# Performance work log

Hardware: AMD Instinct MI355X
Metric: run time of the kernel (lower is better)

The kernel has to match this reference:

```python
import jax, jax.numpy as jnp
import numpy as np

B, S, D, H, G = 16, 512, 1024, 128, 256  # batch, seq, lstm_in, lstm_hidden, gat_dim

def _linear(x, W, b):
    return x @ W.T + b

def _lstm_dir(xs, Wih, Whh, bih, bhh, reverse):
    # xs: [S, B, Din] -> hs: [S, B, H]; PyTorch gate order i, f, g, o
    b = bih + bhh
    def step(carry, xt):
        h, c = carry
        z = xt @ Wih.T + h @ Whh.T + b
        i, f, g, o = jnp.split(z, 4, axis=-1)
        c = jax.nn.sigmoid(f) * c + jax.nn.sigmoid(i) * jnp.tanh(g)
        h = jax.nn.sigmoid(o) * jnp.tanh(c)
        return (h, c), h
    init = (jnp.zeros((xs.shape[1], Whh.shape[1]), xs.dtype),
            jnp.zeros((xs.shape[1], Whh.shape[1]), xs.dtype))
    _, hs = jax.lax.scan(step, init, xs, reverse=reverse)
    return hs

def _forward(x, adj,
             l0f_Wih, l0f_Whh, l0f_bih, l0f_bhh, l0b_Wih, l0b_Whh, l0b_bih, l0b_bhh,
             l1f_Wih, l1f_Whh, l1f_bih, l1f_bhh, l1b_Wih, l1b_Whh, l1b_bih, l1b_bhh,
             fc1_W, fc1_b, wattn_W, wattn_b, lin0_W, lin0_b, lin1_W, lin1_b,
             linf_W, linf_b, fcA_W, fcA_b, fcB_W, fcB_b, fcC_W, fcC_b):
    # ---- 2-layer bidirectional LSTM ----
    xs = jnp.swapaxes(x, 0, 1)  # [S, B, D]
    h0 = jnp.concatenate([_lstm_dir(xs, l0f_Wih, l0f_Whh, l0f_bih, l0f_bhh, False),
                          _lstm_dir(xs, l0b_Wih, l0b_Whh, l0b_bih, l0b_bhh, True)], axis=-1)
    h1 = jnp.concatenate([_lstm_dir(h0, l1f_Wih, l1f_Whh, l1f_bih, l1f_bhh, False),
                          _lstm_dir(h0, l1b_Wih, l1b_Whh, l1b_bih, l1b_bhh, True)], axis=-1)
    out_lstm = jnp.swapaxes(h1, 0, 1)  # [B, S, 2H]
    # ---- GAT on fc1(x) ----
    g = _linear(x, fc1_W, fc1_b)  # [B, S, G]
    idx = jnp.arange(S)
    adj = adj.at[:, idx, idx].set(1.0)
    eye = 1e-05 * jnp.eye(S, dtype=x.dtype)
    for l in range(4):
        g0 = g
        q = _linear(g, wattn_W[l], wattn_b[l])
        a = jax.nn.sigmoid(jnp.einsum('bij,bkj->bik', q, g)) + eye
        a = a * adj
        a = a / jnp.sum(a, axis=2, keepdims=True)
        g = jnp.einsum('bij,bjd->bid', a, g)
        g = jax.nn.relu(_linear(g, lin0_W[l], lin0_b[l]))
        g = jax.nn.relu(_linear(g, lin1_W[l], lin1_b[l]))
        g = g + g0
    g = _linear(g, linf_W, linf_b)
    # ---- head (dropout in eval mode -> identity) ----
    hidden = jnp.mean(jnp.concatenate([out_lstm, g], axis=2), axis=1)  # [B, 512]
    y = jax.nn.leaky_relu(_linear(hidden, fcA_W, fcA_b), 0.1)
    y = jax.nn.leaky_relu(_linear(y, fcB_W, fcB_b), 0.1)
    y = _linear(y, fcC_W, fcC_b)  # [B, 2]
    return y, hidden


def setup_inputs() -> dict:
    key = jax.random.key(0)
    ks = jax.random.split(key, 40)
    r = lambda k, shape: jax.random.normal(k, shape, jnp.float32) * 0.05
    inp = {}
    inp['x'] = jax.random.normal(ks[0], (B, S, D), jnp.float32)
    inp['adj'] = (jax.random.uniform(ks[1], (B, S, S)) < 0.05).astype(jnp.float32)
    # LSTM params: layer0 input D, layer1 input 2H; forward/backward directions
    inp['l0f_Wih'] = r(ks[2], (4 * H, D)); inp['l0f_Whh'] = r(ks[3], (4 * H, H))
    inp['l0f_bih'] = r(ks[4], (4 * H,));  inp['l0f_bhh'] = r(ks[5], (4 * H,))
    inp['l0b_Wih'] = r(ks[6], (4 * H, D)); inp['l0b_Whh'] = r(ks[7], (4 * H, H))
    inp['l0b_bih'] = r(ks[8], (4 * H,));  inp['l0b_bhh'] = r(ks[9], (4 * H,))
    inp['l1f_Wih'] = r(ks[10], (4 * H, 2 * H)); inp['l1f_Whh'] = r(ks[11], (4 * H, H))
    inp['l1f_bih'] = r(ks[12], (4 * H,)); inp['l1f_bhh'] = r(ks[13], (4 * H,))
    inp['l1b_Wih'] = r(ks[14], (4 * H, 2 * H)); inp['l1b_Whh'] = r(ks[15], (4 * H, H))
    inp['l1b_bih'] = r(ks[16], (4 * H,)); inp['l1b_bhh'] = r(ks[17], (4 * H,))
    inp['fc1_W'] = r(ks[18], (G, D)); inp['fc1_b'] = r(ks[19], (G,))
    inp['wattn_W'] = r(ks[20], (4, G, G)); inp['wattn_b'] = r(ks[21], (4, G))
    inp['lin0_W'] = r(ks[22], (4, G, G)); inp['lin0_b'] = r(ks[23], (4, G))
    inp['lin1_W'] = r(ks[24], (4, G, G)); inp['lin1_b'] = r(ks[25], (4, G))
    inp['linf_W'] = r(ks[26], (G, G)); inp['linf_b'] = r(ks[27], (G,))
    inp['fcA_W'] = r(ks[28], (128, 512)); inp['fcA_b'] = r(ks[29], (128,))
    inp['fcB_W'] = r(ks[30], (32, 128)); inp['fcB_b'] = r(ks[31], (32,))
    inp['fcC_W'] = r(ks[32], (2, 32)); inp['fcC_b'] = r(ks[33], (2,))
    return inp


def reference(x, adj,
              l0f_Wih, l0f_Whh, l0f_bih, l0f_bhh, l0b_Wih, l0b_Whh, l0b_bih, l0b_bhh,
              l1f_Wih, l1f_Whh, l1f_bih, l1f_bhh, l1b_Wih, l1b_Whh, l1b_bih, l1b_bhh,
              fc1_W, fc1_b, wattn_W, wattn_b, lin0_W, lin0_b, lin1_W, lin1_b,
              linf_W, linf_b, fcA_W, fcA_b, fcB_W, fcB_b, fcC_W, fcC_b):
    return _forward(x, adj,
                    l0f_Wih, l0f_Whh, l0f_bih, l0f_bhh, l0b_Wih, l0b_Whh, l0b_bih, l0b_bhh,
                    l1f_Wih, l1f_Whh, l1f_bih, l1f_bhh, l1b_Wih, l1b_Whh, l1b_bih, l1b_bhh,
                    fc1_W, fc1_b, wattn_W, wattn_b, lin0_W, lin0_b, lin1_W, lin1_b,
                    linf_W, linf_b, fcA_W, fcA_b, fcB_W, fcB_b, fcC_W, fcC_b)
```

## Files before the change

### kernel.cpp

```cpp
#include <hip/hip_runtime.h>
#include <stdint.h>

#define B_ 16
#define S_ 512
#define D_ 1024
#define H4 512
#define G_ 256

typedef unsigned short u16;
using short8 = __attribute__((ext_vector_type(8))) short;
using f32x4  = __attribute__((ext_vector_type(4))) float;

__device__ __forceinline__ u16 f2bf(float f){
  unsigned int u = __float_as_uint(f);
  u += 0x7fffu + ((u >> 16) & 1u);
  return (u16)(u >> 16);
}
__device__ __forceinline__ float bf2f(u16 h){
  return __uint_as_float(((unsigned int)h) << 16);
}

struct CvtSegs {
  const float4* src[14];
  short4* dst[14];
  int blk0[15];
};
__global__ __launch_bounds__(256) void cvt_multi(CvtSegs cs){
  int blk = blockIdx.x;
  int s = 0;
  #pragma unroll
  for (int k = 0; k < 14; ++k) if (cs.blk0[k + 1] <= blk) s = k + 1;
  int i = (blk - cs.blk0[s]) * 256 + threadIdx.x;
  float4 v = cs.src[s][i];
  short4 o;
  o.x = (short)f2bf(v.x); o.y = (short)f2bf(v.y);
  o.z = (short)f2bf(v.z); o.w = (short)f2bf(v.w);
  cs.dst[s][i] = o;
}

__global__ __launch_bounds__(256) void bias_prep(const float* a,const float* b,const float* c,const float* d,
                                                 const float* e,const float* f,const float* g,const float* h,
                                                 float* out){
  int i = blockIdx.x * 256 + threadIdx.x;
  if (i >= 2048) return;
  int p = i >> 9, k = i & 511;
  const float* x1 = (p==0)?a:(p==1)?c:(p==2)?e:g;
  const float* x2 = (p==0)?b:(p==1)?d:(p==2)?f:h;
  out[i] = x1[k] + x2[k];
}

template<int ACT, bool OUT_BF16, int PERM, bool RESID>
__device__ __forceinline__ void gemm_bt_body(
    const u16* __restrict__ A, const u16* __restrict__ W,
    const float* __restrict__ bias, const u16* __restrict__ resid,
    void* __restrict__ outp, int M, int N, int K,
    long sA, long sW, long sO, int bx, int by, int bz)
{
  const u16* Ab = A + (long)bz * sA;
  const u16* Wb = W + (long)bz * sW;
  const int bm0 = by * 64, bn0 = bx * 64;
  const int tid = threadIdx.x;
  const int l = tid & 63, wid = tid >> 6;
  const int wm = (wid >> 1) * 32, wn = (wid & 1) * 32;
  const int lr = l & 15, lk8 = (l >> 4) * 8;

  const f32x4 z4 = {0.f, 0.f, 0.f, 0.f};
  f32x4 acc[2][2] = {{z4, z4}, {z4, z4}};

  const u16* Ap0 = Ab + (long)(bm0 + wm + lr) * K + lk8;
  const u16* Wp0 = Wb + (long)(bn0 + wn + lr) * K + lk8;
  for (int k0 = 0; k0 < K; k0 += 32) {
    short8 a0 = *reinterpret_cast<const short8*>(Ap0 + k0);
    short8 a1 = *reinterpret_cast<const short8*>(Ap0 + (long)16 * K + k0);
    short8 b0 = *reinterpret_cast<const short8*>(Wp0 + k0);
    short8 b1 = *reinterpret_cast<const short8*>(Wp0 + (long)16 * K + k0);
    acc[0][0] = __builtin_amdgcn_mfma_f32_16x16x32_bf16(a0, b0, acc[0][0], 0, 0, 0);
    acc[0][1] = __builtin_amdgcn_mfma_f32_16x16x32_bf16(a0, b1, acc[0][1], 0, 0, 0);
    acc[1][0] = __builtin_amdgcn_mfma_f32_16x16x32_bf16(a1, b0, acc[1][0], 0, 0, 0);
    acc[1][1] = __builtin_amdgcn_mfma_f32_16x16x32_bf16(a1, b1, acc[1][1], 0, 0, 0);
  }
  #pragma unroll
  for (int mt = 0; mt < 2; ++mt)
  #pragma unroll
  for (int nt = 0; nt < 2; ++nt) {
    int n = bn0 + wn + 16 * nt + lr;
    float bv = bias ? bias[n] : 0.f;
    #pragma unroll
    for (int r = 0; r < 4; ++r) {
      int m = bm0 + wm + 16 * mt + (l >> 4) * 4 + r;
      float v = acc[mt][nt][r] + bv;
      if (ACT == 1) v = fmaxf(v, 0.f);
      if (RESID) v += bf2f(resid[(long)m * N + n]);
      long oi;
      if (PERM == 2) {
        int t = m & 511, b = m >> 9;
        oi = (long)((t * 16 + b) * 128 + (n & 127)) * 4 + (n >> 7);
      } else {
        oi = (long)bz * sO + (long)m * N + n;
      }
      if (OUT_BF16) ((u16*)outp)[oi] = f2bf(v);
      else          ((float*)outp)[oi] = v;
    }
  }
}

template<int ACT, bool OUT_BF16, int PERM, bool RESID>
__global__ __launch_bounds__(256) void gemm_bt(
    const u16* __restrict__ A, const u16* __restrict__ W,
    const float* __restrict__ bias, const u16* __restrict__ resid,
    void* __restrict__ outp, int M, int N, int K,
    long sA, long sW, long sO)
{
  gemm_bt_body<ACT, OUT_BF16, PERM, RESID>(A, W, bias, resid, outp, M, N, K,
                                           sA, sW, sO, blockIdx.x, blockIdx.y, blockIdx.z);
}

__device__ __forceinline__ void gemm_bt_body8(
    const u16* __restrict__ A, const u16* __restrict__ W,
    const float* __restrict__ bias, u16* __restrict__ out,
    int N, int K, int bx, int by)
{
  const int bm0 = by * 64, bn0 = bx * 128;
  const int tid = threadIdx.x;
  const int l = tid & 63, wid = tid >> 6;
  const int wm = (wid >> 2) * 32, wn = (wid & 3) * 32;
  const int lr = l & 15, lk8 = (l >> 4) * 8;

  const f32x4 z4 = {0.f, 0.f, 0.f, 0.f};
  f32x4 acc[2][2] = {{z4, z4}, {z4, z4}};

  const u16* Ap0 = A + (long)(bm0 + wm + lr) * K + lk8;
  const u16* Wp0 = W + (long)(bn0 + wn + lr) * K + lk8;
  for (int k0 = 0; k0 < K; k0 += 32) {
    short8 a0 = *reinterpret_cast<const short8*>(Ap0 + k0);
    short8 a1 = *reinterpret_cast<const short8*>(Ap0 + (long)16 * K + k0);
    short8 b0 = *reinterpret_cast<const short8*>(Wp0 + k0);
    short8 b1 = *reinterpret_cast<const short8*>(Wp0 + (long)16 * K + k0);
    acc[0][0] = __builtin_amdgcn_mfma_f32_16x16x32_bf16(a0, b0, acc[0][0], 0, 0, 0);
    acc[0][1] = __builtin_amdgcn_mfma_f32_16x16x32_bf16(a0, b1, acc[0][1], 0, 0, 0);
    acc[1][0] = __builtin_amdgcn_mfma_f32_16x16x32_bf16(a1, b0, acc[1][0], 0, 0, 0);
    acc[1][1] = __builtin_amdgcn_mfma_f32_16x16x32_bf16(a1, b1, acc[1][1], 0, 0, 0);
  }
  #pragma unroll
  for (int mt = 0; mt < 2; ++mt)
  #pragma unroll
  for (int nt = 0; nt < 2; ++nt) {
    int n = bn0 + wn + 16 * nt + lr;
    float bv = bias[n];
    #pragma unroll
    for (int r = 0; r < 4; ++r) {
      int m = bm0 + wm + 16 * mt + (l >> 4) * 4 + r;
      out[(long)m * N + n] = f2bf(acc[mt][nt][r] + bv);
    }
  }
}

__device__ __forceinline__ void lstm_scan7_body(
    const float* __restrict__ X, const u16* __restrict__ Whh,
    u16* __restrict__ Hout, int dir, int bg)
{
  __shared__ __align__(16) u16 h_lds[16 * 136];
  __shared__ float z_lds[2 * 516];

  const int tid = threadIdx.x;
  const int l = tid & 63, w = tid >> 6;
  const int lr = l & 15, lk = l >> 4;

  short8 bfrag[4][4];
  #pragma unroll
  for (int nt = 0; nt < 4; ++nt)
    #pragma unroll
    for (int ks = 0; ks < 4; ++ks)
      bfrag[nt][ks] = *reinterpret_cast<const short8*>(
          Whh + (64 * w + 16 * nt + lr) * 128 + 32 * ks + 8 * lk);

  for (int i = tid; i < 16 * 136; i += 512) h_lds[i] = 0;

  const int j  = tid & 127;
  const int bq = tid >> 7;
  float c = 0.f;
  float4 xA, xB, xC, xD;

  __syncthreads();

  auto loadX = [&](int t) -> float4 {
    int ta = dir ? (S_ - 1 - t) : t;
    return *reinterpret_cast<const float4*>(X + (size_t)((ta * 16 + bg + bq) * 128 + j) * 4);
  };
  if (bq < 2) { xA = loadX(0); xB = loadX(1); xC = loadX(2); }

  const f32x4 z4 = {0.f, 0.f, 0.f, 0.f};

  auto step = [&](int t, float4& xc, float4& xt, int tload) {
    short8 af[4];
    #pragma unroll
    for (int ks = 0; ks < 4; ++ks)
      af[ks] = *reinterpret_cast<const short8*>(h_lds + lr * 136 + 32 * ks + 8 * lk);
    f32x4 acc[4] = {z4, z4, z4, z4};
    #pragma unroll
    for (int nt = 0; nt < 4; ++nt)
      #pragma unroll
      for (int ks = 0; ks < 4; ++ks)
        acc[nt] = __builtin_amdgcn_mfma_f32_16x16x32_bf16(af[ks], bfrag[nt][ks], acc[nt], 0, 0, 0);
    if (lk == 0) {
      #pragma unroll
      for (int nt = 0; nt < 4; ++nt)
        #pragma unroll
        for (int r = 0; r < 2; ++r)
          z_lds[r * 516 + 64 * w + 16 * nt + lr] = acc[nt][r];
    }
    if (bq < 2 && tload < S_) xt = loadX(tload);
    asm volatile("s_waitcnt lgkmcnt(0)" ::: "memory");
    __builtin_amdgcn_s_barrier();
    if (bq < 2) {
      int ta = dir ? (S_ - 1 - t) : t;
      float zi = z_lds[bq * 516 + j      ] + xc.x;
      float zf = z_lds[bq * 516 + 128 + j] + xc.y;
      float zg = z_lds[bq * 516 + 256 + j] + xc.z;
      float zo = z_lds[bq * 516 + 384 + j] + xc.w;
      float si = __fdividef(1.f, 1.f + __expf(-zi));
      float sf = __fdividef(1.f, 1.f + __expf(-zf));
      float so = __fdividef(1.f, 1.f + __expf(-zo));
      float eg = __expf(2.f * zg);
      float tg = 1.f - __fdividef(2.f, eg + 1.f);
      c = sf * c + si * tg;
      float ec = __expf(2.f * c);
      float tc = 1.f - __fdividef(2.f, ec + 1.f);
      float hv = so * tc;
      u16 hb = f2bf(hv);
      h_lds[bq * 136 + j] = hb;
      Hout[((size_t)(bg + bq) * S_ + ta) * 256 + dir * 128 + j] = hb;
    }
    asm volatile("s_waitcnt lgkmcnt(0)" ::: "memory");
    __builtin_amdgcn_s_barrier();
  };

  for (int t = 0; t < S_; t += 4) {
    step(t,     xA, xD, t + 3);
    step(t + 1, xB, xA, t + 4);
    step(t + 2, xC, xB, t + 5);
    step(t + 3, xD, xC, t + 6);
  }
}

__global__ __launch_bounds__(512, 1) void scan_fused(
    const float* __restrict__ Xf, const float* __restrict__ Xb,
    const u16* __restrict__ Whhf, const u16* __restrict__ Whhb,
    u16* __restrict__ Hout,
    const u16* __restrict__ gA, const u16* __restrict__ gW,
    const float* __restrict__ gb, u16* __restrict__ gOut, int gK)
{
  if (blockIdx.x < 16) {
    int dir = blockIdx.x & 1, bg = (blockIdx.x >> 1) * 2;
    lstm_scan7_body(dir ? Xb : Xf, dir ? Whhb : Whhf, Hout, dir, bg);
  } else {
    int bi = blockIdx.x - 16;
    gemm_bt_body8(gA, gW, gb, gOut, 256, gK, bi & 1, bi >> 1);
  }
}

__global__ __launch_bounds__(256) void attn_norm(
    const float* __restrict__ sc, const float* __restrict__ adj, u16* __restrict__ abf)
{
  int bz = blockIdx.y;
  int i = blockIdx.x * 4 + (threadIdx.x >> 6);
  int l = threadIdx.x & 63;
  const float* srow = sc  + ((long)bz * 512 + i) * 512;
  const float* arow = adj + ((long)bz * 512 + i) * 512;
  float av[8]; float sum = 0.f;
  #pragma unroll
  for (int k = 0; k < 8; ++k) {
    int jj = l + 64 * k;
    float sg = __fdividef(1.f, 1.f + __expf(-srow[jj]));
    float v = (jj == i) ? (sg + 1e-5f) : sg * arow[jj];
    av[k] = v; sum += v;
  }
  #pragma unroll
  for (int off = 32; off; off >>= 1) sum += __shfl_xor(sum, off);
  float r = __fdividef(1.f, sum);
  u16* orow = abf + ((long)bz * 512 + i) * 512;
  #pragma unroll
  for (int k = 0; k < 8; ++k) orow[l + 64 * k] = f2bf(av[k] * r);
}

__global__ __launch_bounds__(256) void transpose_g(const u16* __restrict__ in, u16* __restrict__ out)
{
  __shared__ u16 tile[32][33];
  int bz = blockIdx.z;
  int s0 = blockIdx.x * 32, d0 = blockIdx.y * 32;
  int tx = threadIdx.x & 31, ty = threadIdx.x >> 5;
  const u16* ip = in + (long)bz * 512 * 256;
  u16* op = out + (long)bz * 256 * 512;
  #pragma unroll
  for (int k = 0; k < 32; k += 8) tile[ty + k][tx] = ip[(long)(s0 + ty + k) * 256 + d0 + tx];
  __syncthreads();
  #pragma unroll
  for (int k = 0; k < 32; k += 8) op[(long)(d0 + ty + k) * 512 + s0 + tx] = tile[tx][ty + k];
}

__global__ __launch_bounds__(256) void mean_cat(
    const u16* __restrict__ lstm, const u16* __restrict__ gf, float* __restrict__ dout)
{
  int b = blockIdx.x;
  for (int cc = threadIdx.x; cc < 512; cc += 256) {
    const u16* src = (cc < 256) ? (lstm + (long)b * 512 * 256 + cc)
                                : (gf   + (long)b * 512 * 256 + (cc - 256));
    float s = 0.f;
    for (int t = 0; t < 512; ++t) s += bf2f(src[(long)t * 256]);
    dout[32 + b * 512 + cc] = s * (1.f / 512.f);
  }
}

__global__ __launch_bounds__(256) void head_kernel(
    const float* __restrict__ hidden,
    const float* __restrict__ fcA_W, const float* __restrict__ fcA_b,
    const float* __restrict__ fcB_W, const float* __restrict__ fcB_b,
    const float* __restrict__ fcC_W, const float* __restrict__ fcC_b,
    float* __restrict__ y)
{
  __shared__ float hb[16 * 512];
  __shared__ float ab[16 * 128];
  __shared__ float bb[16 * 32];
  int tid = threadIdx.x;
  for (int i = tid; i < 8192; i += 256) hb[i] = hidden[i];
  __syncthreads();
  for (int o = tid; o < 2048; o += 256) {
    int b = o >> 7, jj = o & 127;
    float acc = fcA_b[jj];
    const float* wrow = fcA_W + jj * 512;
    const float* hrow = hb + b * 512;
    for (int k = 0; k < 512; ++k) acc += hrow[k] * wrow[k];
    ab[o] = acc > 0.f ? acc : 0.1f * acc;
  }
  __syncthreads();
  for (int o = tid; o < 512; o += 256) {
    int b = o >> 5, jj = o & 31;
    float acc = fcB_b[jj];
    for (int k = 0; k < 128; ++k) acc += ab[b * 128 + k] * fcB_W[jj * 128 + k];
    bb[o] = acc > 0.f ? acc : 0.1f * acc;
  }
  __syncthreads();
  if (tid < 32) {
    int b = tid >> 1, jj = tid & 1;
    float acc = fcC_b[jj];
    for (int k = 0; k < 32; ++k) acc += bb[b * 32 + k] * fcC_W[jj * 32 + k];
    y[b * 2 + jj] = acc;
  }
}

extern "C" void kernel_launch(void* const* d_in, const int* in_sizes, int n_in,
                              void* d_out, int out_size, void* d_ws, size_t ws_size,
                              hipStream_t stream)
{
  const float* x       = (const float*)d_in[0];
  const float* adj     = (const float*)d_in[1];
  const float* l0f_Wih = (const float*)d_in[2];
  const float* l0f_Whh = (const float*)d_in[3];
  const float* l0f_bih = (const float*)d_in[4];
  const float* l0f_bhh = (const float*)d_in[5];
  const float* l0b_Wih = (const float*)d_in[6];
  const float* l0b_Whh = (const float*)d_in[7];
  const float* l0b_bih = (const float*)d_in[8];
  const float* l0b_bhh = (const float*)d_in[9];
  const float* l1f_Wih = (const float*)d_in[10];
  const float* l1f_Whh = (const float*)d_in[11];
  const float* l1f_bih = (const float*)d_in[12];
  const float* l1f_bhh = (const float*)d_in[13];
  const float* l1b_Wih = (const float*)d_in[14];
  const float* l1b_Whh = (const float*)d_in[15];
  const float* l1b_bih = (const float*)d_in[16];
  const float* l1b_bhh = (const float*)d_in[17];
  const float* fc1_W   = (const float*)d_in[18];
  const float* fc1_b   = (const float*)d_in[19];
  const float* wattn_W = (const float*)d_in[20];
  const float* wattn_b = (const float*)d_in[21];
  const float* lin0_W  = (const float*)d_in[22];
  const float* lin0_b  = (const float*)d_in[23];
  const float* lin1_W  = (const float*)d_in[24];
  const float* lin1_b  = (const float*)d_in[25];
  const float* linf_W  = (const float*)d_in[26];
  const float* linf_b  = (const float*)d_in[27];
  const float* fcA_W   = (const float*)d_in[28];
  const float* fcA_b   = (const float*)d_in[29];
  const float* fcB_W   = (const float*)d_in[30];
  const float* fcB_b   = (const float*)d_in[31];
  const float* fcC_W   = (const float*)d_in[32];
  const float* fcC_b   = (const float*)d_in[33];

  char* wp = (char*)d_ws;
  auto alloc = [&](size_t n) -> void* { void* p = wp; wp += (n + 255) & ~(size_t)255; return p; };

  u16* x_bf     = (u16*)alloc((size_t)B_ * S_ * D_ * 2);
  u16* w0f_ih   = (u16*)alloc((size_t)512 * 1024 * 2);
  u16* w0b_ih   = (u16*)alloc((size_t)512 * 1024 * 2);
  u16* w1f_ih   = (u16*)alloc((size_t)512 * 256 * 2);
  u16* w1b_ih   = (u16*)alloc((size_t)512 * 256 * 2);
  u16* w0f_hh   = (u16*)alloc((size_t)512 * 128 * 2);
  u16* w0b_hh   = (u16*)alloc((size_t)512 * 128 * 2);
  u16* w1f_hh   = (u16*)alloc((size_t)512 * 128 * 2);
  u16* w1b_hh   = (u16*)alloc((size_t)512 * 128 * 2);
  u16* wfc1     = (u16*)alloc((size_t)256 * 1024 * 2);
  u16* wattn_bf = (u16*)alloc((size_t)4 * 256 * 256 * 2);
  u16* wlin0_bf = (u16*)alloc((size_t)4 * 256 * 256 * 2);
  u16* wlin1_bf = (u16*)alloc((size_t)4 * 256 * 256 * 2);
  u16* wlinf_bf = (u16*)alloc((size_t)256 * 256 * 2);
  float* bias4  = (float*)alloc((size_t)2048 * 4);
  float* X0f    = (float*)alloc((size_t)S_ * 16 * 512 * 4);
  float* X0b    = (float*)alloc((size_t)S_ * 16 * 512 * 4);
  u16* h0       = (u16*)alloc((size_t)B_ * S_ * 256 * 2);
  u16* lstm_out = (u16*)alloc((size_t)B_ * S_ * 256 * 2);
  u16* gA       = (u16*)alloc((size_t)B_ * S_ * 256 * 2);
  u16* gB       = (u16*)alloc((size_t)B_ * S_ * 256 * 2);
  u16* qb       = (u16*)alloc((size_t)B_ * S_ * 256 * 2);
  u16* gT       = (u16*)alloc((size_t)B_ * S_ * 256 * 2);
  u16* t1       = (u16*)alloc((size_t)B_ * S_ * 256 * 2);
  u16* t2       = (u16*)alloc((size_t)B_ * S_ * 256 * 2);
  float* sc     = (float*)alloc((size_t)B_ * S_ * S_ * 4);
  u16* abf      = (u16*)alloc((size_t)B_ * S_ * S_ * 2);

  CvtSegs cs;
  int nb = 0, si = 0;
  auto seg = [&](const float* s, u16* d, int n) {
    cs.src[si] = (const float4*)s; cs.dst[si] = (short4*)d;
    cs.blk0[si] = nb; nb += (n / 4 + 255) / 256; ++si;
  };
  seg(x, x_bf, B_ * S_ * D_);
  seg(l0f_Wih, w0f_ih, 512 * 1024);
  seg(l0b_Wih, w0b_ih, 512 * 1024);
  seg(l1f_Wih, w1f_ih, 512 * 256);
  seg(l1b_Wih, w1b_ih, 512 * 256);
  seg(l0f_Whh, w0f_hh, 512 * 128);
  seg(l0b_Whh, w0b_hh, 512 * 128);
  seg(l1f_Whh, w1f_hh, 512 * 128);
  seg(l1b_Whh, w1b_hh, 512 * 128);
  seg(fc1_W, wfc1, 256 * 1024);
  seg(wattn_W, wattn_bf, 4 * 256 * 256);
  seg(lin0_W, wlin0_bf, 4 * 256 * 256);
  seg(lin1_W, wlin1_bf, 4 * 256 * 256);
  seg(linf_W, wlinf_bf, 256 * 256);
  for (int k = si; k <= 14; ++k) cs.blk0[k] = nb;
  cvt_multi<<<nb, 256, 0, stream>>>(cs);
  bias_prep<<<8, 256, 0, stream>>>(l0f_bih, l0f_bhh, l0b_bih, l0b_bhh,
                                   l1f_bih, l1f_bhh, l1b_bih, l1b_bhh, bias4);

  gemm_bt<0, false, 2, false><<<dim3(8, 128, 1), 256, 0, stream>>>(
      x_bf, w0f_ih, bias4 + 0, nullptr, X0f, 8192, 512, 1024, 0, 0, 0);
  gemm_bt<0, false, 2, false><<<dim3(8, 128, 1), 256, 0, stream>>>(
      x_bf, w0b_ih, bias4 + 512, nullptr, X0b, 8192, 512, 1024, 0, 0, 0);
  scan_fused<<<16 + 256, 512, 0, stream>>>(X0f, X0b, w0f_hh, w0b_hh, h0,
                                           x_bf, wfc1, fc1_b, gA, 1024);
  gemm_bt<0, false, 2, false><<<dim3(8, 128, 1), 256, 0, stream>>>(
      h0, w1f_ih, bias4 + 1024, nullptr, X0f, 8192, 512, 256, 0, 0, 0);
  gemm_bt<0, false, 2, false><<<dim3(8, 128, 1), 256, 0, stream>>>(
      h0, w1b_ih, bias4 + 1536, nullptr, X0b, 8192, 512, 256, 0, 0, 0);
  scan_fused<<<16 + 256, 512, 0, stream>>>(X0f, X0b, w1f_hh, w1b_hh, lstm_out,
                                           gA, wattn_bf, wattn_b, qb, 256);

  u16* gcur = gA; u16* gnext = gB;
  for (int lyr = 0; lyr < 4; ++lyr) {
    if (lyr > 0)
      gemm_bt<0, true, 0, false><<<dim3(4, 128, 1), 256, 0, stream>>>(
          gcur, wattn_bf + lyr * 65536, wattn_b + lyr * 256, nullptr, qb, 8192, 256, 256, 0, 0, 0);
    gemm_bt<0, false, 0, false><<<dim3(8, 8, 16), 256, 0, stream>>>(
        qb, gcur, nullptr, nullptr, sc, 512, 512, 256, 131072, 131072, 262144);
    attn_norm<<<dim3(128, 16), 256, 0, stream>>>(sc, adj, abf);
    transpose_g<<<dim3(16, 8, 16), 256, 0, stream>>>(gcur, gT);
    gemm_bt<0, true, 0, false><<<dim3(4, 8, 16), 256, 0, stream>>>(
        abf, gT, nullptr, nullptr, t1, 512, 256, 512, 262144, 131072, 131072);
    gemm_bt<1, true, 0, false><<<dim3(4, 128, 1), 256, 0, stream>>>(
        t1, wlin0_bf + lyr * 65536, lin0_b + lyr * 256, nullptr, t2, 8192, 256, 256, 0, 0, 0);
    gemm_bt<1, true, 0, true><<<dim3(4, 128, 1), 256, 0, stream>>>(
        t2, wlin1_bf + lyr * 65536, lin1_b + lyr * 256, gcur, gnext, 8192, 256, 256, 0, 0, 0);
    u16* tmp = gcur; gcur = gnext; gnext = tmp;
  }
  gemm_bt<0, true, 0, false><<<dim3(4, 128, 1), 256, 0, stream>>>(
      gcur, wlinf_bf, linf_b, nullptr, t2, 8192, 256, 256, 0, 0, 0);

  mean_cat<<<16, 256, 0, stream>>>(lstm_out, t2, (float*)d_out);
  head_kernel<<<1, 256, 0, stream>>>((const float*)d_out + 32,
                                     fcA_W, fcA_b, fcB_W, fcB_b, fcC_W, fcC_b,
                                     (float*)d_out);
}
```

Measured before the change: 1.360 ms.

## Restructure LSTM scan per batch and fuse GAT attention normalization into GEMMs

The LSTM recurrence now runs one block per batch element and direction, using double-buffered hidden state in shared memory and computing gates straight from MFMA accumulators, which removes the z_lds round trip and one barrier per step. The paired forward and backward input projections are merged into a single launch. In the GAT loop, the sigmoid, adjacency mask and diagonal term are applied in the score GEMM epilogue, so the fp32 score matrix is no longer written and reread. A small row-sum kernel produces inverse sums that the aggregation GEMM applies in its epilogue, and the wattn projection is fused with the transpose into one launch. The row sums are taken from bf16-rounded unnormalized values, which slightly changes numerics, and the scan now has 32 blocks each doing less work per step.

```diff
diff --git a/kernel.cpp b/kernel.cpp
--- a/kernel.cpp
+++ b/kernel.cpp
@@ -49,10 +49,11 @@
   out[i] = x1[k] + x2[k];
 }
 
-template<int ACT, bool OUT_BF16, int PERM, bool RESID>
+template<int EPI, bool OUT_BF16, int PERM, bool RESID>
 __device__ __forceinline__ void gemm_bt_body(
     const u16* __restrict__ A, const u16* __restrict__ W,
     const float* __restrict__ bias, const u16* __restrict__ resid,
+    const float* __restrict__ ex,
     void* __restrict__ outp, int M, int N, int K,
     long sA, long sW, long sO, int bx, int by, int bz)
 {
@@ -89,7 +90,12 @@
     for (int r = 0; r < 4; ++r) {
       int m = bm0 + wm + 16 * mt + (l >> 4) * 4 + r;
       float v = acc[mt][nt][r] + bv;
-      if (ACT == 1) v = fmaxf(v, 0.f);
+      if (EPI == 1) v = fmaxf(v, 0.f);
+      if (EPI == 2) {
+        float sg = __fdividef(1.f, 1.f + __expf(-v));
+        v = (n == m) ? (sg + 1e-5f) : sg * ex[((long)bz * 512 + m) * 512 + n];
+      }
+      if (EPI == 3) v *= ex[(long)bz * 512 + m];
       if (RESID) v += bf2f(resid[(long)m * N + n]);
       long oi;
       if (PERM == 2) {
@@ -104,15 +110,26 @@
   }
 }
 
-template<int ACT, bool OUT_BF16, int PERM, bool RESID>
+template<int EPI, bool OUT_BF16, int PERM, bool RESID>
 __global__ __launch_bounds__(256) void gemm_bt(
     const u16* __restrict__ A, const u16* __restrict__ W,
     const float* __restrict__ bias, const u16* __restrict__ resid,
+    const float* __restrict__ ex,
     void* __restrict__ outp, int M, int N, int K,
     long sA, long sW, long sO)
 {
-  gemm_bt_body<ACT, OUT_BF16, PERM, RESID>(A, W, bias, resid, outp, M, N, K,
+  gemm_bt_body<EPI, OUT_BF16, PERM, RESID>(A, W, bias, resid, ex, outp, M, N, K,
                                            sA, sW, sO, blockIdx.x, blockIdx.y, blockIdx.z);
+}
+
+__global__ __launch_bounds__(256) void proj2(
+    const u16* __restrict__ A, const u16* __restrict__ W0, const u16* __restrict__ W1,
+    const float* __restrict__ bias, float* __restrict__ O0, float* __restrict__ O1, int K)
+{
+  int z = blockIdx.z;
+  gemm_bt_body<0, false, 2, false>(A, z ? W1 : W0, bias + z * 512, nullptr, nullptr,
+                                   z ? O1 : O0, 8192, 512, K, 0, 0, 0,
+                                   blockIdx.x, blockIdx.y, 0);
 }
 
 __device__ __forceinline__ void gemm_bt_body8(
@@ -155,12 +172,11 @@
   }
 }
 
-__device__ __forceinline__ void lstm_scan7_body(
+__device__ __forceinline__ void lstm_scan8_body(
     const float* __restrict__ X, const u16* __restrict__ Whh,
-    u16* __restrict__ Hout, int dir, int bg)
-{
-  __shared__ __align__(16) u16 h_lds[16 * 136];
-  __shared__ float z_lds[2 * 516];
+    u16* __restrict__ Hout, int dir, int bat)
+{
+  __shared__ __align__(16) u16 hbuf[2][16][136];
 
   const int tid = threadIdx.x;
   const int l = tid & 63, w = tid >> 6;
@@ -168,56 +184,43 @@
 
   short8 bfrag[4][4];
   #pragma unroll
-  for (int nt = 0; nt < 4; ++nt)
+  for (int g = 0; g < 4; ++g)
     #pragma unroll
     for (int ks = 0; ks < 4; ++ks)
-      bfrag[nt][ks] = *reinterpret_cast<const short8*>(
-          Whh + (64 * w + 16 * nt + lr) * 128 + 32 * ks + 8 * lk);
-
-  for (int i = tid; i < 16 * 136; i += 512) h_lds[i] = 0;
-
-  const int j  = tid & 127;
-  const int bq = tid >> 7;
+      bfrag[g][ks] = *reinterpret_cast<const short8*>(
+          Whh + (g * 128 + 16 * w + lr) * 128 + 32 * ks + 8 * lk);
+
+  for (int i = tid; i < 2 * 16 * 136; i += 512) ((u16*)hbuf)[i] = 0;
+
   float c = 0.f;
+  const f32x4 z4 = {0.f, 0.f, 0.f, 0.f};
+
+  auto ldX = [&](int t) -> float4 {
+    int ta = dir ? (S_ - 1 - t) : t;
+    return *reinterpret_cast<const float4*>(X + (size_t)((ta * 16 + bat) * 128 + 16 * w + lr) * 4);
+  };
   float4 xA, xB, xC, xD;
-
+  if (lk == 0) { xA = ldX(0); xB = ldX(1); xC = ldX(2); }
   __syncthreads();
 
-  auto loadX = [&](int t) -> float4 {
-    int ta = dir ? (S_ - 1 - t) : t;
-    return *reinterpret_cast<const float4*>(X + (size_t)((ta * 16 + bg + bq) * 128 + j) * 4);
-  };
-  if (bq < 2) { xA = loadX(0); xB = loadX(1); xC = loadX(2); }
-
-  const f32x4 z4 = {0.f, 0.f, 0.f, 0.f};
-
   auto step = [&](int t, float4& xc, float4& xt, int tload) {
+    const int p = t & 1;
     short8 af[4];
     #pragma unroll
     for (int ks = 0; ks < 4; ++ks)
-      af[ks] = *reinterpret_cast<const short8*>(h_lds + lr * 136 + 32 * ks + 8 * lk);
+      af[ks] = *reinterpret_cast<const short8*>(&hbuf[p][lr][32 * ks + 8 * lk]);
     f32x4 acc[4] = {z4, z4, z4, z4};
     #pragma unroll
-    for (int nt = 0; nt < 4; ++nt)
+    for (int g = 0; g < 4; ++g)
       #pragma unroll
       for (int ks = 0; ks < 4; ++ks)
-        acc[nt] = __builtin_amdgcn_mfma_f32_16x16x32_bf16(af[ks], bfrag[nt][ks], acc[nt], 0, 0, 0);
+        acc[g] = __builtin_amdgcn_mfma_f32_16x16x32_bf16(af[ks], bfrag[g][ks], acc[g], 0, 0, 0);
     if (lk == 0) {
-      #pragma unroll
-      for (int nt = 0; nt < 4; ++nt)
-        #pragma unroll
-        for (int r = 0; r < 2; ++r)
-          z_lds[r * 516 + 64 * w + 16 * nt + lr] = acc[nt][r];
-    }
-    if (bq < 2 && tload < S_) xt = loadX(tload);
-    asm volatile("s_waitcnt lgkmcnt(0)" ::: "memory");
-    __builtin_amdgcn_s_barrier();
-    if (bq < 2) {
-      int ta = dir ? (S_ - 1 - t) : t;
-      float zi = z_lds[bq * 516 + j      ] + xc.x;
-      float zf = z_lds[bq * 516 + 128 + j] + xc.y;
-      float zg = z_lds[bq * 516 + 256 + j] + xc.z;
-      float zo = z_lds[bq * 516 + 384 + j] + xc.w;
+      if (tload < S_) xt = ldX(tload);
+      float zi = acc[0][0] + xc.x;
+      float zf = acc[1][0] + xc.y;
+      float zg = acc[2][0] + xc.z;
+      float zo = acc[3][0] + xc.w;
       float si = __fdividef(1.f, 1.f + __expf(-zi));
       float sf = __fdividef(1.f, 1.f + __expf(-zf));
       float so = __fdividef(1.f, 1.f + __expf(-zo));
@@ -226,10 +229,10 @@
       c = sf * c + si * tg;
       float ec = __expf(2.f * c);
       float tc = 1.f - __fdividef(2.f, ec + 1.f);
-      float hv = so * tc;
-      u16 hb = f2bf(hv);
-      h_lds[bq * 136 + j] = hb;
-      Hout[((size_t)(bg + bq) * S_ + ta) * 256 + dir * 128 + j] = hb;
+      u16 hb = f2bf(so * tc);
+      int ta = dir ? (S_ - 1 - t) : t;
+      hbuf[p ^ 1][0][16 * w + lr] = hb;
+      Hout[((size_t)bat * S_ + ta) * 256 + dir * 128 + 16 * w + lr] = hb;
     }
     asm volatile("s_waitcnt lgkmcnt(0)" ::: "memory");
     __builtin_amdgcn_s_barrier();
@@ -250,44 +253,19 @@
     const u16* __restrict__ gA, const u16* __restrict__ gW,
     const float* __restrict__ gb, u16* __restrict__ gOut, int gK)
 {
-  if (blockIdx.x < 16) {
-    int dir = blockIdx.x & 1, bg = (blockIdx.x >> 1) * 2;
-    lstm_scan7_body(dir ? Xb : Xf, dir ? Whhb : Whhf, Hout, dir, bg);
+  if (blockIdx.x < 32) {
+    int dir = blockIdx.x & 1, bat = blockIdx.x >> 1;
+    lstm_scan8_body(dir ? Xb : Xf, dir ? Whhb : Whhf, Hout, dir, bat);
   } else {
-    int bi = blockIdx.x - 16;
+    int bi = blockIdx.x - 32;
     gemm_bt_body8(gA, gW, gb, gOut, 256, gK, bi & 1, bi >> 1);
   }
 }
 
-__global__ __launch_bounds__(256) void attn_norm(
-    const float* __restrict__ sc, const float* __restrict__ adj, u16* __restrict__ abf)
-{
-  int bz = blockIdx.y;
-  int i = blockIdx.x * 4 + (threadIdx.x >> 6);
-  int l = threadIdx.x & 63;
-  const float* srow = sc  + ((long)bz * 512 + i) * 512;
-  const float* arow = adj + ((long)bz * 512 + i) * 512;
-  float av[8]; float sum = 0.f;
-  #pragma unroll
-  for (int k = 0; k < 8; ++k) {
-    int jj = l + 64 * k;
-    float sg = __fdividef(1.f, 1.f + __expf(-srow[jj]));
-    float v = (jj == i) ? (sg + 1e-5f) : sg * arow[jj];
-    av[k] = v; sum += v;
-  }
-  #pragma unroll
-  for (int off = 32; off; off >>= 1) sum += __shfl_xor(sum, off);
-  float r = __fdividef(1.f, sum);
-  u16* orow = abf + ((long)bz * 512 + i) * 512;
-  #pragma unroll
-  for (int k = 0; k < 8; ++k) orow[l + 64 * k] = f2bf(av[k] * r);
-}
-
-__global__ __launch_bounds__(256) void transpose_g(const u16* __restrict__ in, u16* __restrict__ out)
+__device__ __forceinline__ void transpose_body(const u16* __restrict__ in, u16* __restrict__ out,
+                                               int bz, int s0, int d0)
 {
   __shared__ u16 tile[32][33];
-  int bz = blockIdx.z;
-  int s0 = blockIdx.x * 32, d0 = blockIdx.y * 32;
   int tx = threadIdx.x & 31, ty = threadIdx.x >> 5;
   const u16* ip = in + (long)bz * 512 * 256;
   u16* op = out + (long)bz * 256 * 512;
@@ -296,6 +274,40 @@
   __syncthreads();
   #pragma unroll
   for (int k = 0; k < 32; k += 8) op[(long)(d0 + ty + k) * 512 + s0 + tx] = tile[tx][ty + k];
+}
+
+__global__ __launch_bounds__(256) void transpose_g(const u16* __restrict__ in, u16* __restrict__ out)
+{
+  transpose_body(in, out, blockIdx.z, blockIdx.x * 32, blockIdx.y * 32);
+}
+
+__global__ __launch_bounds__(256) void wattn_trans(
+    const u16* __restrict__ gcur, const u16* __restrict__ wW, const float* __restrict__ wb,
+    u16* __restrict__ qb, u16* __restrict__ gT)
+{
+  if (blockIdx.x < 512) {
+    int b = blockIdx.x;
+    gemm_bt_body<0, true, 0, false>(gcur, wW, wb, nullptr, nullptr, qb,
+                                    8192, 256, 256, 0, 0, 0, b & 3, b >> 2, 0);
+  } else {
+    int b = blockIdx.x - 512;
+    int bz = b >> 7, rem = b & 127;
+    transpose_body(gcur, gT, bz, (rem & 15) * 32, (rem >> 4) * 32);
+  }
+}
+
+__global__ __launch_bounds__(256) void rowsum_inv(const u16* __restrict__ abf, float* __restrict__ rinv)
+{
+  int bz = blockIdx.y;
+  int row = blockIdx.x * 4 + (threadIdx.x >> 6);
+  int l = threadIdx.x & 63;
+  short8 v = *reinterpret_cast<const short8*>(abf + ((size_t)bz * 512 + row) * 512 + l * 8);
+  float s = 0.f;
+  #pragma unroll
+  for (int k = 0; k < 8; ++k) s += bf2f((u16)v[k]);
+  #pragma unroll
+  for (int off = 32; off; off >>= 1) s += __shfl_xor(s, off);
+  if (l == 0) rinv[bz * 512 + row] = __fdividef(1.f, s);
 }
 
 __global__ __launch_bounds__(256) void mean_cat(
@@ -415,8 +427,8 @@
   u16* gT       = (u16*)alloc((size_t)B_ * S_ * 256 * 2);
   u16* t1       = (u16*)alloc((size_t)B_ * S_ * 256 * 2);
   u16* t2       = (u16*)alloc((size_t)B_ * S_ * 256 * 2);
-  float* sc     = (float*)alloc((size_t)B_ * S_ * S_ * 4);
   u16* abf      = (u16*)alloc((size_t)B_ * S_ * S_ * 2);
+  float* rinv   = (float*)alloc((size_t)B_ * S_ * 4);
 
   CvtSegs cs;
   int nb = 0, si = 0;
@@ -443,38 +455,33 @@
   bias_prep<<<8, 256, 0, stream>>>(l0f_bih, l0f_bhh, l0b_bih, l0b_bhh,
                                    l1f_bih, l1f_bhh, l1b_bih, l1b_bhh, bias4);
 
-  gemm_bt<0, false, 2, false><<<dim3(8, 128, 1), 256, 0, stream>>>(
-      x_bf, w0f_ih, bias4 + 0, nullptr, X0f, 8192, 512, 1024, 0, 0, 0);
-  gemm_bt<0, false, 2, false><<<dim3(8, 128, 1), 256, 0, stream>>>(
-      x_bf, w0b_ih, bias4 + 512, nullptr, X0b, 8192, 512, 1024, 0, 0, 0);
-  scan_fused<<<16 + 256, 512, 0, stream>>>(X0f, X0b, w0f_hh, w0b_hh, h0,
+  proj2<<<dim3(8, 128, 2), 256, 0, stream>>>(x_bf, w0f_ih, w0b_ih, bias4, X0f, X0b, 1024);
+  scan_fused<<<32 + 256, 512, 0, stream>>>(X0f, X0b, w0f_hh, w0b_hh, h0,
                                            x_bf, wfc1, fc1_b, gA, 1024);
-  gemm_bt<0, false, 2, false><<<dim3(8, 128, 1), 256, 0, stream>>>(
-      h0, w1f_ih, bias4 + 1024, nullptr, X0f, 8192, 512, 256, 0, 0, 0);
-  gemm_bt<0, false, 2, false><<<dim3(8, 128, 1), 256, 0, stream>>>(
-      h0, w1b_ih, bias4 + 1536, nullptr, X0b, 8192, 512, 256, 0, 0, 0);
-  scan_fused<<<16 + 256, 512, 0, stream>>>(X0f, X0b, w1f_hh, w1b_hh, lstm_out,
+  proj2<<<dim3(8, 128, 2), 256, 0, stream>>>(h0, w1f_ih, w1b_ih, bias4 + 1024, X0f, X0b, 256);
+  scan_fused<<<32 + 256, 512, 0, stream>>>(X0f, X0b, w1f_hh, w1b_hh, lstm_out,
                                            gA, wattn_bf, wattn_b, qb, 256);
 
   u16* gcur = gA; u16* gnext = gB;
   for (int lyr = 0; lyr < 4; ++lyr) {
-    if (lyr > 0)
-      gemm_bt<0, true, 0, false><<<dim3(4, 128, 1), 256, 0, stream>>>(
-          gcur, wattn_bf + lyr * 65536, wattn_b + lyr * 256, nullptr, qb, 8192, 256, 256, 0, 0, 0);
-    gemm_bt<0, false, 0, false><<<dim3(8, 8, 16), 256, 0, stream>>>(
-        qb, gcur, nullptr, nullptr, sc, 512, 512, 256, 131072, 131072, 262144);
-    attn_norm<<<dim3(128, 16), 256, 0, stream>>>(sc, adj, abf);
-    transpose_g<<<dim3(16, 8, 16), 256, 0, stream>>>(gcur, gT);
-    gemm_bt<0, true, 0, false><<<dim3(4, 8, 16), 256, 0, stream>>>(
-        abf, gT, nullptr, nullptr, t1, 512, 256, 512, 262144, 131072, 131072);
+    if (lyr == 0)
+      transpose_g<<<dim3(16, 8, 16), 256, 0, stream>>>(gcur, gT);
+    else
+      wattn_trans<<<512 + 2048, 256, 0, stream>>>(gcur, wattn_bf + lyr * 65536,
+                                                  wattn_b + lyr * 256, qb, gT);
+    gemm_bt<2, true, 0, false><<<dim3(8, 8, 16), 256, 0, stream>>>(
+        qb, gcur, nullptr, nullptr, adj, abf, 512, 512, 256, 131072, 131072, 262144);
+    rowsum_inv<<<dim3(128, 16), 256, 0, stream>>>(abf, rinv);
+    gemm_bt<3, true, 0, false><<<dim3(4, 8, 16), 256, 0, stream>>>(
+        abf, gT, nullptr, nullptr, rinv, t1, 512, 256, 512, 262144, 131072, 131072);
     gemm_bt<1, true, 0, false><<<dim3(4, 128, 1), 256, 0, stream>>>(
-        t1, wlin0_bf + lyr * 65536, lin0_b + lyr * 256, nullptr, t2, 8192, 256, 256, 0, 0, 0);
+        t1, wlin0_bf + lyr * 65536, lin0_b + lyr * 256, nullptr, nullptr, t2, 8192, 256, 256, 0, 0, 0);
     gemm_bt<1, true, 0, true><<<dim3(4, 128, 1), 256, 0, stream>>>(
-        t2, wlin1_bf + lyr * 65536, lin1_b + lyr * 256, gcur, gnext, 8192, 256, 256, 0, 0, 0);
+        t2, wlin1_bf + lyr * 65536, lin1_b + lyr * 256, gcur, nullptr, gnext, 8192, 256, 256, 0, 0, 0);
     u16* tmp = gcur; gcur = gnext; gnext = tmp;
   }
   gemm_bt<0, true, 0, false><<<dim3(4, 128, 1), 256, 0, stream>>>(
-      gcur, wlinf_bf, linf_b, nullptr, t2, 8192, 256, 256, 0, 0, 0);
+      gcur, wlinf_bf, linf_b, nullptr, nullptr, t2, 8192, 256, 256, 0, 0, 0);
 
   mean_cat<<<16, 256, 0, stream>>>(lstm_out, t2, (float*)d_out);
   head_kernel<<<1, 256, 0, stream>>>((const float*)d_out + 32,
```

Measured after the change: 1.231 ms. -9.4%, faster.
